# Kernel optimization log

Hardware: AMD Instinct MI355X
Metric: run time of the kernel (lower is better)

The kernel has to match this reference:

```python
import jax, jax.numpy as jnp
import numpy as np

B, DIM, N_TREES, DEPTH, UNITS = 512, 256, 512, 6, 3
N_LEAVES = 2 ** DEPTH


def binary_lookup_table(depth):
    # (depth, 2**depth, 2) float table of leaf bit codes, as in get_binary_lookup_table
    idx = np.arange(2 ** depth)
    off = 2 ** np.arange(depth)
    bits = (idx[None, :] // off[:, None]) % 2  # (depth, 2**depth)
    lut = np.stack([bits, 1 - bits], axis=-1).astype(np.float32)
    return jnp.asarray(lut)


def sparsemax(z, axis):
    # sparsemax along `axis` (Martins & Astudillo 2016)
    z = jnp.moveaxis(z, axis, -1)
    K = z.shape[-1]
    zs = jnp.flip(jnp.sort(z, axis=-1), axis=-1)
    k = jnp.arange(1, K + 1, dtype=z.dtype)
    cum = jnp.cumsum(zs, axis=-1)
    support = (1.0 + k * zs) > cum
    k_z = jnp.sum(support, axis=-1, keepdims=True)  # int
    tau_num = jnp.take_along_axis(cum, k_z - 1, axis=-1) - 1.0
    tau = tau_num / k_z.astype(z.dtype)
    out = jnp.maximum(z - tau, 0.0)
    return jnp.moveaxis(out, -1, axis)


def sparsemoid(t):
    return jnp.clip(0.5 * t + 0.5, 0.0, 1.0)


def setup_inputs() -> dict:
    key = jax.random.key(0)
    k1, k2, k3, k4 = jax.random.split(key, 4)
    return {
        "x": jax.random.normal(k1, (B, DIM), dtype=jnp.float32),
        "feature_selection_logits": jax.random.normal(k2, (DIM, N_TREES, DEPTH), dtype=jnp.float32),
        "feature_thresholds": jax.random.normal(k3, (N_TREES, DEPTH), dtype=jnp.float32) * 0.5,
        "log_temperatures": jnp.zeros((N_TREES, DEPTH), dtype=jnp.float32),
        "response": jax.random.normal(k4, (N_TREES, UNITS, N_LEAVES), dtype=jnp.float32),
    }


def reference(x, feature_selection_logits, feature_thresholds, log_temperatures, response):
    depth = feature_thresholds.shape[-1]
    lut = binary_lookup_table(depth)  # (d, 2**d, 2) constant
    # soft feature selection: sparsemax over the feature dimension i
    selectors = sparsemax(feature_selection_logits, axis=0)  # (i, n, d)
    fv = jnp.einsum('bi,ind->bnd', x, selectors)  # (b, n, d)
    # binary gates
    tl = (fv - feature_thresholds) * jnp.exp(-log_temperatures)  # (b, n, d)
    gates = sparsemoid(jnp.stack([-tl, tl], axis=-1))  # (b, n, d, 2)
    # leaf aggregation: product over depth of per-level gate selected by the leaf bit code
    agg = jnp.einsum('bnds,dcs->bndc', gates, lut)  # (b, n, d, 2**d)
    leaf_probs = jnp.prod(agg, axis=-2)  # (b, n, 2**d)
    out = jnp.einsum('bnc,nuc->bnu', leaf_probs, response)  # (b, n, units)
    return out
```

## Files before the change

kernel.cpp:

```cpp
#include <hip/hip_runtime.h>
#include <hip/hip_bf16.h>

#define BATCH 512
#define DIM 256
#define NT 512
#define DEPTH 6
#define UNITS 3
#define NL 64
#define COLS (NT * DEPTH)
#define KMAX 32


__global__ __launch_bounds__(256) void k_prep(
    const float* __restrict__ logits, const float* __restrict__ resp,
    int2* __restrict__ lists, int* __restrict__ cnt,
    float4* __restrict__ resp4) {
  if (blockIdx.x >= 768) {
    int idx = (blockIdx.x - 768) * 256 + threadIdx.x;
    int n = idx / (UNITS * NL);
    int r = idx % (UNITS * NL);
    int u = r / NL, c = r % NL;
    ((float*)&resp4[c * NT + n])[u] = resp[idx];
    return;
  }
  const int wv = threadIdx.x >> 6, lane = threadIdx.x & 63;
  const int col = blockIdx.x * 4 + wv;
  const int n = col / DEPTH, d = col % DEPTH;

  float z[4];
#pragma unroll
  for (int j = 0; j < 4; ++j) z[j] = logits[(j * 64 + lane) * COLS + col];

  float m = fmaxf(fmaxf(z[0], z[1]), fmaxf(z[2], z[3]));
#pragma unroll
  for (int o = 32; o > 0; o >>= 1) m = fmaxf(m, __shfl_xor(m, o, 64));

  float tau = m - 1.0f;
  for (int it = 0; it < 16; ++it) {
    float s = 0.0f, k = 0.0f;
#pragma unroll
    for (int j = 0; j < 4; ++j) {
      float dd = z[j] - tau;
      if (dd > 0.0f) { s += dd; k += 1.0f; }
    }
#pragma unroll
    for (int o = 32; o > 0; o >>= 1) {
      s += __shfl_xor(s, o, 64);
      k += __shfl_xor(k, o, 64);
    }
    float delta = (s - 1.0f) / k;
    tau += delta;
    if (fabsf(delta) < 1e-7f) break;
  }

  int base = 0;
#pragma unroll
  for (int j = 0; j < 4; ++j) {
    bool nz = z[j] > tau;
    unsigned long long mk = __ballot(nz);
    int pos = base + __popcll(mk & ((1ull << lane) - 1ull));
    if (nz && pos < KMAX)
      lists[(d * KMAX + pos) * NT + n] =
          make_int2(j * 64 + lane, __float_as_int(z[j] - tau));
    base += __popcll(mk);
  }
  if (lane == 0) cnt[d * NT + n] = min(base, KMAX);
}

__global__ __launch_bounds__(256) void k_forest3(
    const float* __restrict__ x, const int2* __restrict__ lists,
    const int* __restrict__ cnt, const float* __restrict__ thr,
    const float* __restrict__ ltemp, const float4* __restrict__ resp4,
    float* __restrict__ out) {
  const int tid = threadIdx.x;
  const int nloc = tid & 63, bg = tid >> 6;
  const int tt = blockIdx.x & 7, bt = blockIdx.x >> 3;
  const int n = tt * 64 + nloc;
  const int b0 = bt * 8;

  __shared__ float xl[8 * DIM];
#pragma unroll
  for (int k = 0; k < 8; ++k) xl[k * 256 + tid] = x[b0 * DIM + k * 256 + tid];
  __syncthreads();

  const float* xr0 = &xl[(bg * 2 + 0) * DIM];
  const float* xr1 = &xl[(bg * 2 + 1) * DIM];

  float fv0[DEPTH], fv1[DEPTH];
#pragma unroll
  for (int d = 0; d < DEPTH; ++d) { fv0[d] = 0.0f; fv1[d] = 0.0f; }

#pragma unroll
  for (int d = 0; d < DEPTH; ++d) {
    const int c = cnt[d * NT + n];
    for (int j = 0; j < c; ++j) {
      int2 e = lists[(d * KMAX + j) * NT + n];
      float v = __int_as_float(e.y);
      fv0[d] = fmaf(v, xr0[e.x], fv0[d]);
      fv1[d] = fmaf(v, xr1[e.x], fv1[d]);
    }
  }

  float th[DEPTH], et[DEPTH];
#pragma unroll
  for (int d = 0; d < DEPTH; ++d) {
    th[d] = thr[n * DEPTH + d];
    et[d] = expf(-ltemp[n * DEPTH + d]);
  }

  float t012[2][8], t345[2][8];
#pragma unroll
  for (int r = 0; r < 2; ++r) {
    float g0[DEPTH], g1[DEPTH];
#pragma unroll
    for (int d = 0; d < DEPTH; ++d) {
      float av = r ? fv1[d] : fv0[d];
      float tl = (av - th[d]) * et[d];
      float gg = fminf(fmaxf(0.5f * tl + 0.5f, 0.0f), 1.0f);
      g0[d] = gg;
      g1[d] = 1.0f - gg;
    }
#pragma unroll
    for (int c = 0; c < 8; ++c) {
      t012[r][c] = ((c & 1) ? g1[0] : g0[0]) * ((c & 2) ? g1[1] : g0[1]) *
                   ((c & 4) ? g1[2] : g0[2]);
      t345[r][c] = ((c & 1) ? g1[3] : g0[3]) * ((c & 2) ? g1[4] : g0[4]) *
                   ((c & 4) ? g1[5] : g0[5]);
    }
  }

  float o00 = 0, o01 = 0, o02 = 0, o10 = 0, o11 = 0, o12 = 0;
#pragma unroll
  for (int c = 0; c < NL; ++c) {
    float4 rr = resp4[c * NT + n];
    float p0 = t012[0][c & 7] * t345[0][c >> 3];
    float p1 = t012[1][c & 7] * t345[1][c >> 3];
    o00 = fmaf(p0, rr.x, o00); o01 = fmaf(p0, rr.y, o01); o02 = fmaf(p0, rr.z, o02);
    o10 = fmaf(p1, rr.x, o10); o11 = fmaf(p1, rr.y, o11); o12 = fmaf(p1, rr.z, o12);
  }

  const int ba = b0 + bg * 2, bb = ba + 1;
  float* oa = out + ((size_t)ba * NT + n) * UNITS;
  float* ob = out + ((size_t)bb * NT + n) * UNITS;
  oa[0] = o00; oa[1] = o01; oa[2] = o02;
  ob[0] = o10; ob[1] = o11; ob[2] = o12;
}

extern "C" void kernel_launch(void* const* d_in, const int* in_sizes, int n_in,
                              void* d_out, int out_size, void* d_ws, size_t ws_size,
                              hipStream_t stream) {
  const float* x    = (const float*)d_in[0];
  const float* fsl  = (const float*)d_in[1];
  const float* thr  = (const float*)d_in[2];
  const float* lt   = (const float*)d_in[3];
  const float* resp = (const float*)d_in[4];
  float* out = (float*)d_out;

  int2* lists = (int2*)d_ws;
  int* cnt = (int*)(lists + DEPTH * KMAX * NT);
  float4* resp4 =
      (float4*)((char*)d_ws + DEPTH * KMAX * NT * 8 + DEPTH * NT * 4);

  k_prep<<<768 + 384, 256, 0, stream>>>(fsl, resp, lists, cnt, resp4);
  k_forest3<<<512, 256, 0, stream>>>(x, lists, cnt, thr, lt, resp4, out);
}
```

Baseline: 99.90 us.

## Transpose logits, pack sparse lists into float4/byte-index quads, predigest thresholds

Adds a pack kernel that transposes the selection logits through shared memory, so the sparsemax kernel can read each column contiguously instead of with a large stride. It also precomputes thresholds and exp(-log temperature) into depth-major arrays. Sparse selector lists are stored as float4 values with four byte indices packed into one uint, padded with zeros, and the forest kernel loops over quads up to the wave-wide maximum count. This gives wider, coalesced loads and uniform loop trip counts, at the cost of an extra kernel launch and the transposed-logits buffer round trip.

Result: faster. 94.23 us (-5.7%).

```diff
diff --git a/kernel.cpp b/kernel.cpp
--- a/kernel.cpp
+++ b/kernel.cpp
@@ -11,25 +11,50 @@
 #define KMAX 32
 
 
-__global__ __launch_bounds__(256) void k_prep(
+__global__ __launch_bounds__(256) void k_pack(
     const float* __restrict__ logits, const float* __restrict__ resp,
-    int2* __restrict__ lists, int* __restrict__ cnt,
-    float4* __restrict__ resp4) {
-  if (blockIdx.x >= 768) {
-    int idx = (blockIdx.x - 768) * 256 + threadIdx.x;
+    const float* __restrict__ thr, const float* __restrict__ ltemp,
+    float* __restrict__ logitsT, float4* __restrict__ resp4,
+    float* __restrict__ pth, float* __restrict__ pet) {
+  const int bid = blockIdx.x, tid = threadIdx.x;
+  if (bid < 192) {
+    const int c0 = (bid % 48) * 64, r0 = (bid / 48) * 64;
+    __shared__ float tile[64][65];
+#pragma unroll
+    for (int e = tid; e < 4096; e += 256) {
+      int r = e >> 6, c = e & 63;
+      tile[r][c] = logits[(r0 + r) * COLS + c0 + c];
+    }
+    __syncthreads();
+#pragma unroll
+    for (int e = tid; e < 4096; e += 256) {
+      int c = e >> 6, r = e & 63;
+      logitsT[(c0 + c) * DIM + r0 + r] = tile[r][c];
+    }
+  } else if (bid < 576) {
+    int idx = (bid - 192) * 256 + tid;
     int n = idx / (UNITS * NL);
     int r = idx % (UNITS * NL);
     int u = r / NL, c = r % NL;
     ((float*)&resp4[c * NT + n])[u] = resp[idx];
-    return;
-  }
+  } else {
+    int idx = (bid - 576) * 256 + tid;
+    int n = idx / DEPTH, d = idx % DEPTH;
+    pth[d * NT + n] = thr[idx];
+    pet[d * NT + n] = expf(-ltemp[idx]);
+  }
+}
+
+__global__ __launch_bounds__(256) void k_sel(
+    const float* __restrict__ logitsT, float4* __restrict__ val4,
+    unsigned int* __restrict__ idx4, int* __restrict__ cnt) {
   const int wv = threadIdx.x >> 6, lane = threadIdx.x & 63;
   const int col = blockIdx.x * 4 + wv;
   const int n = col / DEPTH, d = col % DEPTH;
 
   float z[4];
 #pragma unroll
-  for (int j = 0; j < 4; ++j) z[j] = logits[(j * 64 + lane) * COLS + col];
+  for (int j = 0; j < 4; ++j) z[j] = logitsT[col * DIM + j * 64 + lane];
 
   float m = fmaxf(fmaxf(z[0], z[1]), fmaxf(z[2], z[3]));
 #pragma unroll
@@ -53,25 +78,35 @@
     if (fabsf(delta) < 1e-7f) break;
   }
 
+  float* vbase = (float*)val4;
+  unsigned char* ibase = (unsigned char*)idx4;
   int base = 0;
 #pragma unroll
   for (int j = 0; j < 4; ++j) {
     bool nz = z[j] > tau;
     unsigned long long mk = __ballot(nz);
     int pos = base + __popcll(mk & ((1ull << lane) - 1ull));
-    if (nz && pos < KMAX)
-      lists[(d * KMAX + pos) * NT + n] =
-          make_int2(j * 64 + lane, __float_as_int(z[j] - tau));
+    if (nz && pos < KMAX) {
+      int slot = ((d * 8 + (pos >> 2)) * NT + n) * 4 + (pos & 3);
+      vbase[slot] = z[j] - tau;
+      ibase[slot] = (unsigned char)(j * 64 + lane);
+    }
     base += __popcll(mk);
   }
-  if (lane == 0) cnt[d * NT + n] = min(base, KMAX);
-}
-
-__global__ __launch_bounds__(256) void k_forest3(
-    const float* __restrict__ x, const int2* __restrict__ lists,
-    const int* __restrict__ cnt, const float* __restrict__ thr,
-    const float* __restrict__ ltemp, const float4* __restrict__ resp4,
-    float* __restrict__ out) {
+  const int cc = min(base, KMAX);
+  if (lane >= cc && lane < KMAX) {
+    int slot = ((d * 8 + (lane >> 2)) * NT + n) * 4 + (lane & 3);
+    vbase[slot] = 0.0f;
+    ibase[slot] = 0;
+  }
+  if (lane == 0) cnt[d * NT + n] = cc;
+}
+
+__global__ __launch_bounds__(256) void k_forest4(
+    const float* __restrict__ x, const float4* __restrict__ val4,
+    const unsigned int* __restrict__ idx4, const int* __restrict__ cnt,
+    const float* __restrict__ pth, const float* __restrict__ pet,
+    const float4* __restrict__ resp4, float* __restrict__ out) {
   const int tid = threadIdx.x;
   const int nloc = tid & 63, bg = tid >> 6;
   const int tt = blockIdx.x & 7, bt = blockIdx.x >> 3;
@@ -92,20 +127,30 @@
 
 #pragma unroll
   for (int d = 0; d < DEPTH; ++d) {
-    const int c = cnt[d * NT + n];
-    for (int j = 0; j < c; ++j) {
-      int2 e = lists[(d * KMAX + j) * NT + n];
-      float v = __int_as_float(e.y);
-      fv0[d] = fmaf(v, xr0[e.x], fv0[d]);
-      fv1[d] = fmaf(v, xr1[e.x], fv1[d]);
+    int mc = cnt[d * NT + n];
+#pragma unroll
+    for (int o = 32; o > 0; o >>= 1) mc = max(mc, __shfl_xor(mc, o, 64));
+    const int nq = (mc + 3) >> 2;
+#pragma unroll
+    for (int jq = 0; jq < 8; ++jq) {
+      if (jq < nq) {
+        float4 v = val4[(d * 8 + jq) * NT + n];
+        unsigned int ip = idx4[(d * 8 + jq) * NT + n];
+        int i0 = ip & 255, i1 = (ip >> 8) & 255;
+        int i2 = (ip >> 16) & 255, i3 = ip >> 24;
+        fv0[d] = fmaf(v.x, xr0[i0], fv0[d]); fv1[d] = fmaf(v.x, xr1[i0], fv1[d]);
+        fv0[d] = fmaf(v.y, xr0[i1], fv0[d]); fv1[d] = fmaf(v.y, xr1[i1], fv1[d]);
+        fv0[d] = fmaf(v.z, xr0[i2], fv0[d]); fv1[d] = fmaf(v.z, xr1[i2], fv1[d]);
+        fv0[d] = fmaf(v.w, xr0[i3], fv0[d]); fv1[d] = fmaf(v.w, xr1[i3], fv1[d]);
+      }
     }
   }
 
   float th[DEPTH], et[DEPTH];
 #pragma unroll
   for (int d = 0; d < DEPTH; ++d) {
-    th[d] = thr[n * DEPTH + d];
-    et[d] = expf(-ltemp[n * DEPTH + d]);
+    th[d] = pth[d * NT + n];
+    et[d] = pet[d * NT + n];
   }
 
   float t012[2][8], t345[2][8];
@@ -156,11 +201,16 @@
   const float* resp = (const float*)d_in[4];
   float* out = (float*)d_out;
 
-  int2* lists = (int2*)d_ws;
-  int* cnt = (int*)(lists + DEPTH * KMAX * NT);
-  float4* resp4 =
-      (float4*)((char*)d_ws + DEPTH * KMAX * NT * 8 + DEPTH * NT * 4);
-
-  k_prep<<<768 + 384, 256, 0, stream>>>(fsl, resp, lists, cnt, resp4);
-  k_forest3<<<512, 256, 0, stream>>>(x, lists, cnt, thr, lt, resp4, out);
-}
+  float* ws = (float*)d_ws;
+  float*        logitsT = ws;
+  float4*       resp4   = (float4*)(ws + 786432);
+  float4*       val4    = (float4*)(ws + 917504);
+  unsigned int* idx4    = (unsigned int*)(ws + 1015808);
+  int*          cnt     = (int*)(ws + 1040384);
+  float*        pth     = ws + 1043456;
+  float*        pet     = ws + 1046528;
+
+  k_pack<<<588, 256, 0, stream>>>(fsl, resp, thr, lt, logitsT, resp4, pth, pet);
+  k_sel<<<COLS / 4, 256, 0, stream>>>(logitsT, val4, idx4, cnt);
+  k_forest4<<<512, 256, 0, stream>>>(x, val4, idx4, cnt, pth, pet, resp4, out);
+}
```
